# Optimization experiments

Measured on AMD Instinct MI355X. Metric: run time of the kernel, lower is better.

Reference implementation:

```python
import jax, jax.numpy as jnp
import numpy as np

F_DIM = 128; HID = 32; C = 8 * HID; DEPTH = 5; K = 3; HEADS = 8
JK_H = (7 * C) // 2  # 896, PyG JumpingKnowledge('lstm', C, jk_depth=7)
FLEX = 512; CLASSES = 10; GATE_H = 21 * HID
BS = 512; NPG = 23; N_NODES = BS * NPG
EPS = 1e-5


def _bn(x, gamma=None, beta=None):
    # training-mode BatchNorm1d (biased variance), affine optional
    mu = x.mean(0)
    var = x.var(0)
    y = (x - mu) * jax.lax.rsqrt(var + EPS)
    return y * gamma + beta if gamma is not None else y


def _lstm(seq, w_ih, w_hh, b_ih, b_hh):
    # seq: [T, N, C] -> hidden states [T, N, H]; torch gate order i,f,g,o
    n = seq.shape[1]
    hdim = w_hh.shape[1]
    def step(carry, xt):
        h, c = carry
        z = xt @ w_ih.T + h @ w_hh.T + b_ih + b_hh
        i, f, g, o = jnp.split(z, 4, axis=-1)
        c = jax.nn.sigmoid(f) * c + jax.nn.sigmoid(i) * jnp.tanh(g)
        h = jax.nn.sigmoid(o) * jnp.tanh(c)
        return (h, c), h
    init = (jnp.zeros((n, hdim), seq.dtype), jnp.zeros((n, hdim), seq.dtype))
    _, hs = jax.lax.scan(step, init, seq)
    return hs


def _forward(x, conv1_w, conv1_b, bn1_g, bn1_b, ll1_w, ll1_b, tag_w, tag_b,
             gat_w, gat_asrc, gat_adst, gat_b,
             lw_ih_f, lw_hh_f, lb_ih_f, lb_hh_f, lw_ih_b, lw_hh_b, lb_ih_b, lb_hh_b,
             jk_w, jk_b, fff_w1, fff_b1, fff_w2, fff_b2,
             gate_w1, gate_b1, gate_w2, gate_b2,
             conv2_w, conv2_b, bn2_g, bn2_b, fc_w, fc_b,
             edge_index, batch, num_graphs):
    n, f = x.shape
    bs = num_graphs
    # --- temporal preprocessing: PE over node axis (d_model=23), Conv1d, BN ---
    xt = x.reshape(bs, NPG, f).transpose(0, 2, 1)            # [bs, F, 23]
    pos = jnp.arange(f, dtype=x.dtype)[:, None]
    div = jnp.exp(jnp.arange(0, NPG, 2, dtype=x.dtype) * (-np.log(10000.0) / NPG))
    pe = jnp.zeros((f, NPG), x.dtype)
    pe = pe.at[:, 0::2].set(jnp.sin(pos * div))
    pe = pe.at[:, 1::2].set(jnp.cos(pos * div)[:, :(NPG - 1) // 2])
    xt = (xt + pe[None]).transpose(0, 2, 1)                  # [bs, 23, F]
    xt = jax.lax.conv_general_dilated(xt, conv1_w, (1,), [(1, 1)],
            dimension_numbers=('NCH', 'OIH', 'NCH')) + conv1_b[None, :, None]
    h = _bn(xt.reshape(n, f), bn1_g, bn1_b) @ ll1_w + ll1_b  # [N, HID]
    # --- symmetric gcn_norm (no self loops) shared by all TAGConv layers ---
    src, dst = edge_index[0], edge_index[1]
    deg = jax.ops.segment_sum(jnp.ones(src.shape, h.dtype), dst, n)
    dinv = jnp.where(deg > 0, jax.lax.rsqrt(jnp.maximum(deg, 1.0)), 0.0)
    wnorm = dinv[src] * dinv[dst]                            # [E]
    # GAT uses self loops
    loop = jnp.arange(n, dtype=src.dtype)
    src_sl = jnp.concatenate([src, loop])
    dst_sl = jnp.concatenate([dst, loop])

    jk_seq = []
    for i in range(DEPTH):
        # TAGConv: concat powers of normalized adjacency, then linear
        xs = h
        feats = [h]
        for _ in range(K):
            xs = jax.ops.segment_sum(wnorm[:, None] * xs[src], dst, n)
            feats.append(xs)
        tag = jnp.concatenate(feats, axis=-1) @ tag_w[i] + tag_b[i]
        h = _bn(h + tag)                                     # SublayerConnection (BN affine=False)
        # GATConv, heads=8, concat
        g = (h @ gat_w[i]).reshape(n, HEADS, HID)
        a = jax.nn.leaky_relu((g * gat_asrc[i]).sum(-1)[src_sl]
                              + (g * gat_adst[i]).sum(-1)[dst_sl], 0.2)  # [E', heads]
        m = jax.lax.stop_gradient(jax.ops.segment_max(a, dst_sl, n))
        ea = jnp.exp(a - m[dst_sl])
        alpha = ea / jax.ops.segment_sum(ea, dst_sl, n)[dst_sl]
        out = jax.ops.segment_sum(alpha[:, :, None] * g[src_sl], dst_sl, n)
        jk_seq.append(out.reshape(n, C) + gat_b[i])

    # JumpingKnowledge 'lstm': bi-LSTM attention over the DEPTH layer outputs
    seq = jnp.stack(jk_seq, axis=0)                          # [T=5, N, C]
    hf = _lstm(seq, lw_ih_f, lw_hh_f, lb_ih_f, lb_hh_f)
    hb = _lstm(seq[::-1], lw_ih_b, lw_hh_b, lb_ih_b, lb_hh_b)[::-1]
    att = (jnp.concatenate([hf, hb], -1) @ jk_w + jk_b)[..., 0]  # [T, N]
    w_jk = jax.nn.softmax(att, axis=0)                       # softmax over layers
    xg = (seq * w_jk[:, :, None]).sum(0)                     # [N, C]
    # FinalFeedForward + residual BN (slc4)
    ff = jax.nn.elu(xg @ fff_w1 + fff_b1) @ fff_w2 + fff_b2
    xg = _bn(xg + ff)
    # GlobalAttention pooling per graph
    gate = ((xg @ gate_w1 + gate_b1) @ gate_w2 + gate_b2)[:, 0]  # [N]
    gm = jax.lax.stop_gradient(jax.ops.segment_max(gate, batch, bs))
    ge = jnp.exp(gate - gm[batch])
    gw = ge / jax.ops.segment_sum(ge, batch, bs)[batch]
    pooled = jax.ops.segment_sum(gw[:, None] * xg, batch, bs)    # [bs, C]
    # Conv1d(1->10, k=9) over channel axis, mean over out-channels, BN, classifier
    y = jax.lax.conv_general_dilated(pooled[:, None, :], conv2_w, (1,), [(4, 4)],
            dimension_numbers=('NCH', 'OIH', 'NCH')) + conv2_b[None, :, None]
    y = _bn(y.mean(axis=1), bn2_g, bn2_b)
    return jax.nn.log_softmax(y @ fc_w + fc_b, axis=1)


def setup_inputs() -> dict:
    key = jax.random.key(0)
    it = iter(jax.random.split(key, 48))
    def rn(shape, scale=0.05):
        return jax.random.normal(next(it), shape, dtype=jnp.float32) * scale
    # complete digraph (no self loops) inside each 23-node graph
    s, d = np.meshgrid(np.arange(NPG), np.arange(NPG), indexing='ij')
    mask = s != d
    s, d = s[mask], d[mask]
    off = (np.arange(BS) * NPG)[:, None]
    src = (off + s[None, :]).reshape(-1)
    dst = (off + d[None, :]).reshape(-1)
    edge_index = jnp.asarray(np.stack([src, dst]), dtype=jnp.int32)
    batch = jnp.repeat(jnp.arange(BS, dtype=jnp.int32), NPG)
    return dict(
        x=rn((N_NODES, F_DIM), 1.0),
        edge_index=edge_index, batch=batch, num_graphs=BS,
        conv1_w=rn((NPG, NPG, 3)), conv1_b=rn((NPG,)),
        bn1_g=jnp.ones((F_DIM,), jnp.float32), bn1_b=jnp.zeros((F_DIM,), jnp.float32),
        ll1_w=rn((F_DIM, HID)), ll1_b=rn((HID,)),
        tag_w=rn((DEPTH, (K + 1) * HID, HID)), tag_b=rn((DEPTH, HID)),
        gat_w=rn((DEPTH, HID, HEADS * HID)), gat_asrc=rn((DEPTH, HEADS, HID)),
        gat_adst=rn((DEPTH, HEADS, HID)), gat_b=rn((DEPTH, HEADS * HID)),
        lw_ih_f=rn((4 * JK_H, C)), lw_hh_f=rn((4 * JK_H, JK_H)),
        lb_ih_f=rn((4 * JK_H,)), lb_hh_f=rn((4 * JK_H,)),
        lw_ih_b=rn((4 * JK_H, C)), lw_hh_b=rn((4 * JK_H, JK_H)),
        lb_ih_b=rn((4 * JK_H,)), lb_hh_b=rn((4 * JK_H,)),
        jk_w=rn((2 * JK_H, 1)), jk_b=rn((1,)),
        fff_w1=rn((C, FLEX)), fff_b1=rn((FLEX,)),
        fff_w2=rn((FLEX, C)), fff_b2=rn((C,)),
        gate_w1=rn((C, GATE_H)), gate_b1=rn((GATE_H,)),
        gate_w2=rn((GATE_H, 1)), gate_b2=rn((1,)),
        conv2_w=rn((10, 1, 9)), conv2_b=rn((10,)),
        bn2_g=jnp.ones((C,), jnp.float32), bn2_b=jnp.zeros((C,), jnp.float32),
        fc_w=rn((C, CLASSES)), fc_b=rn((CLASSES,)),
    )


def reference(x, edge_index, batch, num_graphs, conv1_w, conv1_b, bn1_g, bn1_b,
              ll1_w, ll1_b, tag_w, tag_b, gat_w, gat_asrc, gat_adst, gat_b,
              lw_ih_f, lw_hh_f, lb_ih_f, lb_hh_f, lw_ih_b, lw_hh_b, lb_ih_b, lb_hh_b,
              jk_w, jk_b, fff_w1, fff_b1, fff_w2, fff_b2,
              gate_w1, gate_b1, gate_w2, gate_b2,
              conv2_w, conv2_b, bn2_g, bn2_b, fc_w, fc_b):
    return _forward(x, conv1_w, conv1_b, bn1_g, bn1_b, ll1_w, ll1_b, tag_w, tag_b,
                    gat_w, gat_asrc, gat_adst, gat_b,
                    lw_ih_f, lw_hh_f, lb_ih_f, lb_hh_f, lw_ih_b, lw_hh_b, lb_ih_b, lb_hh_b,
                    jk_w, jk_b, fff_w1, fff_b1, fff_w2, fff_b2,
                    gate_w1, gate_b1, gate_w2, gate_b2,
                    conv2_w, conv2_b, bn2_g, bn2_b, fc_w, fc_b,
                    edge_index, batch, num_graphs)
```

## Files before the change

### kernel.cpp

```cpp
#include <hip/hip_runtime.h>
#include <math.h>

#define NNODES 11776
#define NGR    512
#define NPG    23
#define FDIM   128
#define HID    32
#define CDIM   256
#define JKH    896
#define ZCOLS  3584
#define EPSBN  1e-5f

typedef long long i64;
typedef unsigned short ushort_t;
typedef __attribute__((ext_vector_type(8))) short bf16x8;
typedef __attribute__((ext_vector_type(4))) float f32x4;

__device__ __forceinline__ float fsig(float x) { return 1.f / (1.f + __expf(-x)); }
__device__ __forceinline__ float ftanh(float x) {
  x = fminf(fmaxf(x, -15.f), 15.f);
  float e = __expf(2.f * x);
  return (e - 1.f) / (e + 1.f);
}

__device__ __forceinline__ ushort_t f2bf(float x) {
  unsigned u = __float_as_uint(x);
  return (ushort_t)((u + 0x7fffu + ((u >> 16) & 1u)) >> 16);
}
__device__ __forceinline__ float bf2f(ushort_t b) {
  return __uint_as_float(((unsigned)b) << 16);
}

__device__ __forceinline__ void gload16(const ushort_t* g, ushort_t* l) {
  __builtin_amdgcn_global_load_lds(
      (const __attribute__((address_space(1))) void*)g,
      (__attribute__((address_space(3))) void*)l, 16, 0, 0);
}

__global__ __launch_bounds__(256) void conv1_kernel(
    const float* __restrict__ x, const float* __restrict__ w,
    const float* __restrict__ bias, float* __restrict__ out,
    float* __restrict__ stats) {
  int b = blockIdx.x;
  __shared__ float in[NPG][FDIM];
  __shared__ float wsh[NPG * NPG * 3];
  __shared__ float cs[FDIM], cq[FDIM];
  int tid = threadIdx.x;
  if (tid < FDIM) { cs[tid] = 0.f; cq[tid] = 0.f; }
  const float c0 = -2.f * logf(10000.f) / 23.f;
  for (int idx = tid; idx < NPG * FDIM; idx += 256) {
    int p = idx >> 7, f = idx & 127;
    int j = p >> 1;
    float ang = (float)f * expf(c0 * (float)j);
    float pe = (p & 1) ? cosf(ang) : sinf(ang);
    in[p][f] = x[(i64)(b * NPG + p) * FDIM + f] + pe;
  }
  for (int idx = tid; idx < NPG * NPG * 3; idx += 256) wsh[idx] = w[idx];
  __syncthreads();
  float ls = 0.f, lq = 0.f;
  int fme = tid & 127;
  for (int idx = tid; idx < NPG * FDIM; idx += 256) {
    int o = idx >> 7, f = idx & 127;
    float acc = bias[o];
    for (int i = 0; i < NPG; ++i) {
      const float* wr = &wsh[(o * NPG + i) * 3];
      float s = in[i][f] * wr[1];
      if (f > 0)   s += in[i][f - 1] * wr[0];
      if (f < 127) s += in[i][f + 1] * wr[2];
      acc += s;
    }
    out[(i64)(b * NPG + o) * FDIM + f] = acc;
    ls += acc; lq += acc * acc;
  }
  atomicAdd(&cs[fme], ls);
  atomicAdd(&cq[fme], lq);
  __syncthreads();
  if (tid < FDIM) {
    atomicAdd(&stats[tid], cs[tid]);
    atomicAdd(&stats[FDIM + tid], cq[tid]);
  }
}

__global__ __launch_bounds__(256) void col_stats(
    const float* __restrict__ X, int rows, int cols, float* __restrict__ acc) {
  int rpt = 256 / cols;
  int c = threadIdx.x % cols;
  int rsub = threadIdx.x / cols;
  float s = 0.f, q = 0.f;
  for (int r0 = blockIdx.x * rpt; r0 < rows; r0 += gridDim.x * rpt) {
    int r = r0 + rsub;
    if (r < rows) {
      float v = X[(i64)r * cols + c];
      s += v; q += v * v;
    }
  }
  __shared__ float sh[256];
  sh[threadIdx.x] = s;
  __syncthreads();
  if (threadIdx.x < cols) {
    float t = 0.f;
    for (int g = 0; g < rpt; ++g) t += sh[g * cols + c];
    atomicAdd(&acc[c], t);
  }
  __syncthreads();
  sh[threadIdx.x] = q;
  __syncthreads();
  if (threadIdx.x < cols) {
    float t = 0.f;
    for (int g = 0; g < rpt; ++g) t += sh[g * cols + c];
    atomicAdd(&acc[cols + c], t);
  }
}

__global__ __launch_bounds__(256) void fold_ll1(
    const float* __restrict__ acc, const float* __restrict__ g,
    const float* __restrict__ be, const float* __restrict__ w,
    const float* __restrict__ lb, float* __restrict__ Wp, float* __restrict__ bp) {
  int tid = threadIdx.x;
  const float invR = 1.f / (float)NNODES;
  for (int idx = tid; idx < FDIM * HID; idx += 256) {
    int k = idx >> 5;
    float mu = acc[k] * invR;
    float var = acc[FDIM + k] * invR - mu * mu;
    float scale = g[k] * rsqrtf(var + EPSBN);
    Wp[idx] = scale * w[idx];
  }
  if (tid < HID) {
    float s = lb[tid];
    for (int k = 0; k < FDIM; ++k) {
      float mu = acc[k] * invR;
      float var = acc[FDIM + k] * invR - mu * mu;
      float scale = g[k] * rsqrtf(var + EPSBN);
      s += (be[k] - mu * scale) * w[k * HID + tid];
    }
    bp[tid] = s;
  }
}

template <int BT>
__global__ __launch_bounds__(256) void sgemm(
    const float* __restrict__ A, const float* __restrict__ B, float* __restrict__ C,
    int M, int N, int K,
    const float* __restrict__ bias, const float* __restrict__ resid,
    int act, int accumulate) {
  __shared__ float As[16][128];
  __shared__ float Bs[16][128];
  int tid = threadIdx.x;
  int bm0 = blockIdx.x * 128;
  int bn0 = blockIdx.y * 128;
  int tx = tid & 15, ty = tid >> 4;
  float acc[8][8];
#pragma unroll
  for (int i = 0; i < 8; ++i)
#pragma unroll
    for (int j = 0; j < 8; ++j) acc[i][j] = 0.f;

  int ar = tid >> 2;
  int akc = (tid & 3) << 2;
  bool bfull = (bn0 + 127 < N);

  for (int k0 = 0; k0 < K; k0 += 16) {
    {
      const float* ap = A + (i64)(bm0 + ar) * K + k0 + akc;
      float4 a0 = *(const float4*)ap;
      float4 a1 = *(const float4*)(ap + (i64)64 * K);
      As[akc + 0][ar] = a0.x; As[akc + 1][ar] = a0.y;
      As[akc + 2][ar] = a0.z; As[akc + 3][ar] = a0.w;
      As[akc + 0][ar + 64] = a1.x; As[akc + 1][ar + 64] = a1.y;
      As[akc + 2][ar + 64] = a1.z; As[akc + 3][ar + 64] = a1.w;
    }
    if (BT) {
      int br = tid >> 1;
      int bkc = (tid & 1) << 3;
      const float* bp = B + (i64)(bn0 + br) * K + k0 + bkc;
      float4 b0 = *(const float4*)bp;
      float4 b1 = *(const float4*)(bp + 4);
      Bs[bkc + 0][br] = b0.x; Bs[bkc + 1][br] = b0.y;
      Bs[bkc + 2][br] = b0.z; Bs[bkc + 3][br] = b0.w;
      Bs[bkc + 4][br] = b1.x; Bs[bkc + 5][br] = b1.y;
      Bs[bkc + 6][br] = b1.z; Bs[bkc + 7][br] = b1.w;
    } else {
      int bk = tid >> 4;
      int bn = (tid & 15) << 3;
      const float* bp = B + (i64)(k0 + bk) * N + bn0 + bn;
      if (bfull) {
        *(float4*)&Bs[bk][bn] = *(const float4*)bp;
        *(float4*)&Bs[bk][bn + 4] = *(const float4*)(bp + 4);
      } else {
#pragma unroll
        for (int q = 0; q < 8; ++q)
          Bs[bk][bn + q] = (bn0 + bn + q < N) ? bp[q] : 0.f;
      }
    }
    __syncthreads();
#pragma unroll
    for (int kk = 0; kk < 16; ++kk) {
      float a[8], b[8];
      *(float4*)(a)     = *(const float4*)&As[kk][ty * 8];
      *(float4*)(a + 4) = *(const float4*)&As[kk][ty * 8 + 4];
      *(float4*)(b)     = *(const float4*)&Bs[kk][tx * 8];
      *(float4*)(b + 4) = *(const float4*)&Bs[kk][tx * 8 + 4];
#pragma unroll
      for (int i = 0; i < 8; ++i)
#pragma unroll
        for (int j = 0; j < 8; ++j)
          acc[i][j] = fmaf(a[i], b[j], acc[i][j]);
    }
    __syncthreads();
  }
#pragma unroll
  for (int i = 0; i < 8; ++i) {
    int m = bm0 + ty * 8 + i;
#pragma unroll
    for (int j = 0; j < 8; ++j) {
      int n = bn0 + tx * 8 + j;
      if (n < N) {
        i64 ci = (i64)m * N + n;
        float v = acc[i][j];
        if (accumulate) {
          C[ci] += v;
        } else {
          if (bias) v += bias[n];
          if (act == 1) v = v > 0.f ? v : expm1f(v);
          if (resid) v += resid[ci];
          C[ci] = v;
        }
      }
    }
  }
}

__global__ __launch_bounds__(256) void tag_fused(
    const float* __restrict__ hbuf, const float* __restrict__ tag_w,
    const float* __restrict__ tag_b, float* __restrict__ hres,
    float* __restrict__ stats) {
  int b = blockIdx.x, tid = threadIdx.x;
  __shared__ float fe[NPG][FDIM];
  __shared__ float wsh[FDIM * HID];
  __shared__ float S[HID];
  __shared__ float cs[HID], cq[HID];
  if (tid < HID) { cs[tid] = 0.f; cq[tid] = 0.f; }
  const float* hp = hbuf + (i64)b * NPG * HID;
  for (int idx = tid; idx < NPG * HID; idx += 256) fe[idx >> 5][idx & 31] = hp[idx];
  for (int idx = tid; idx < FDIM * HID; idx += 256) wsh[idx] = tag_w[idx];
  __syncthreads();
  if (tid < HID) {
    float s = 0.f;
    for (int p = 0; p < NPG; ++p) s += fe[p][tid];
    S[tid] = s;
  }
  __syncthreads();
  const float wn = 1.f / 22.f;
  for (int idx = tid; idx < NPG * HID; idx += 256) {
    int p = idx >> 5, c = idx & 31;
    float f0 = fe[p][c], Sc = S[c];
    float f1 = (Sc - f0) * wn;
    float f2 = (Sc - f1) * wn;
    float f3 = (Sc - f2) * wn;
    fe[p][HID + c] = f1;
    fe[p][2 * HID + c] = f2;
    fe[p][3 * HID + c] = f3;
  }
  __syncthreads();
  for (int idx = tid; idx < NPG * HID; idx += 256) {
    int p = idx >> 5, c = idx & 31;
    float acc = tag_b[c];
#pragma unroll 8
    for (int k = 0; k < FDIM; ++k) acc += fe[p][k] * wsh[k * HID + c];
    float v = fe[p][c] + acc;
    hres[(i64)(b * NPG + p) * HID + c] = v;
    atomicAdd(&cs[c], v);
    atomicAdd(&cq[c], v * v);
  }
  __syncthreads();
  if (tid < HID) {
    atomicAdd(&stats[tid], cs[tid]);
    atomicAdd(&stats[HID + tid], cq[tid]);
  }
}

__global__ __launch_bounds__(256) void gat_tag_fused(
    const float* __restrict__ hres, const float* __restrict__ stats,
    const float* __restrict__ gat_w, const float* __restrict__ asrc,
    const float* __restrict__ adst, const float* __restrict__ gbias,
    ushort_t* __restrict__ outseq,
    const float* __restrict__ tag_w_next, const float* __restrict__ tag_b_next,
    float* __restrict__ hres_out, float* __restrict__ stats_next, int has_next) {
  int b = blockIdx.x, tid = threadIdx.x;
  __shared__ float hn[NPG * HID];
  __shared__ float ssrc[NPG * 8], sdst[NPG * 8], sinv[NPG * 8];
  __shared__ float buf[10120];
  __shared__ float S[HID], cs[HID], cq[HID];
  float* gsh = buf;
  float* ealpha = buf + 5888;
  const float invR = 1.f / (float)NNODES;
  for (int idx = tid; idx < NPG * HID; idx += 256) {
    int c = idx & 31;
    float mu = stats[c] * invR;
    float var = stats[HID + c] * invR - mu * mu;
    hn[idx] = (hres[(i64)b * NPG * HID + idx] - mu) * rsqrtf(var + EPSBN);
  }
  __syncthreads();
  for (int idx = tid; idx < NPG * CDIM; idx += 256) {
    int p = idx >> 8, d = idx & 255;
    float acc = 0.f;
#pragma unroll
    for (int k = 0; k < HID; ++k) acc += hn[p * HID + k] * gat_w[k * CDIM + d];
    gsh[idx] = acc;
  }
  __syncthreads();
  if (tid < NPG * 8) {
    int p = tid >> 3, hd = tid & 7;
    float s1 = 0.f, s2 = 0.f;
    const float* gp = &gsh[p * CDIM + hd * 32];
#pragma unroll
    for (int d = 0; d < 32; ++d) {
      s1 += gp[d] * asrc[hd * 32 + d];
      s2 += gp[d] * adst[hd * 32 + d];
    }
    ssrc[tid] = s1;
    sdst[tid] = s2;
  }
  __syncthreads();
  if (tid < NPG * 8) {
    int v = tid >> 3, hd = tid & 7;
    float sd = sdst[v * 8 + hd];
    float e[NPG];
    float m = -1e30f;
#pragma unroll
    for (int u = 0; u < NPG; ++u) {
      float xv = ssrc[u * 8 + hd] + sd;
      xv = xv > 0.f ? xv : 0.2f * xv;
      e[u] = xv;
      m = fmaxf(m, xv);
    }
    float s = 0.f;
#pragma unroll
    for (int u = 0; u < NPG; ++u) {
      float t = __expf(e[u] - m);
      ealpha[(v * NPG + u) * 8 + hd] = t;
      s += t;
    }
    sinv[tid] = 1.f / s;
  }
  __syncthreads();
  {
    int hd = tid >> 5, d = tid & 31;
    const i64 base = (i64)b * NPG * CDIM;
    for (int v = 0; v < NPG; ++v) {
      float acc = 0.f;
#pragma unroll
      for (int u = 0; u < NPG; ++u)
        acc += ealpha[(v * NPG + u) * 8 + hd] * gsh[u * CDIM + hd * 32 + d];
      outseq[base + (i64)v * CDIM + hd * 32 + d] =
          f2bf(acc * sinv[v * 8 + hd] + gbias[hd * 32 + d]);
    }
  }
  if (!has_next) return;
  __syncthreads();
  float* fe = buf;
  float* wsh = buf + 2944;
  if (tid < HID) { cs[tid] = 0.f; cq[tid] = 0.f; }
  for (int idx = tid; idx < FDIM * HID; idx += 256) wsh[idx] = tag_w_next[idx];
  for (int idx = tid; idx < NPG * HID; idx += 256)
    fe[(idx >> 5) * FDIM + (idx & 31)] = hn[idx];
  __syncthreads();
  if (tid < HID) {
    float s = 0.f;
    for (int p = 0; p < NPG; ++p) s += fe[p * FDIM + tid];
    S[tid] = s;
  }
  __syncthreads();
  const float wn = 1.f / 22.f;
  for (int idx = tid; idx < NPG * HID; idx += 256) {
    int p = idx >> 5, c = idx & 31;
    float f0 = fe[p * FDIM + c], Sc = S[c];
    float f1 = (Sc - f0) * wn;
    float f2 = (Sc - f1) * wn;
    float f3 = (Sc - f2) * wn;
    fe[p * FDIM + HID + c] = f1;
    fe[p * FDIM + 2 * HID + c] = f2;
    fe[p * FDIM + 3 * HID + c] = f3;
  }
  __syncthreads();
  for (int idx = tid; idx < NPG * HID; idx += 256) {
    int p = idx >> 5, c = idx & 31;
    float acc = tag_b_next[c];
#pragma unroll 8
    for (int k = 0; k < FDIM; ++k) acc += fe[p * FDIM + k] * wsh[k * HID + c];
    float v = fe[p * FDIM + c] + acc;
    hres_out[(i64)(b * NPG + p) * HID + c] = v;
    atomicAdd(&cs[c], v);
    atomicAdd(&cq[c], v * v);
  }
  __syncthreads();
  if (tid < HID) {
    atomicAdd(&stats_next[tid], cs[tid]);
    atomicAdd(&stats_next[HID + tid], cq[tid]);
  }
}

__global__ void pack_w(const float* __restrict__ w, ushort_t* __restrict__ wp,
                       int ldK) {
  i64 total = (i64)ZCOLS * ldK;
  i64 idx = (i64)blockIdx.x * 256 + threadIdx.x;
  i64 stride = (i64)gridDim.x * 256;
  for (; idx < total; idx += stride) {
    int r = (int)(idx / ldK), k = (int)(idx % ldK);
    int g = r / JKH, jj = r % JKH;
    int p = (jj >> 4) * 64 + g * 16 + (jj & 15);
    wp[(i64)p * ldK + k] = f2bf(w[idx]);
  }
}

__global__ void pack_b(const float* __restrict__ a, const float* __restrict__ b,
                       float* __restrict__ bp) {
  int r = blockIdx.x * 256 + threadIdx.x;
  if (r < ZCOLS) {
    int g = r / JKH, jj = r % JKH;
    int p = (jj >> 4) * 64 + g * 16 + (jj & 15);
    bp[p] = a[r] + b[r];
  }
}

__global__ void pack_t(const float* __restrict__ w, ushort_t* __restrict__ wt,
                       int K, int N) {
  i64 total = (i64)K * N;
  i64 idx = (i64)blockIdx.x * 256 + threadIdx.x;
  i64 stride = (i64)gridDim.x * 256;
  for (; idx < total; idx += stride) {
    int k = (int)(idx / N), n = (int)(idx % N);
    wt[(i64)n * K + k] = f2bf(w[idx]);
  }
}

template <int HASH>
__global__ __launch_bounds__(256) void lstm_step(
    const ushort_t* __restrict__ Aseq,
    const ushort_t* __restrict__ Wih,
    const ushort_t* __restrict__ Hprev,
    const ushort_t* __restrict__ Whh,
    const float*  __restrict__ bspk,
    float* __restrict__ Cst,
    ushort_t* __restrict__ Hout,
    const float* __restrict__ jkw,
    float* __restrict__ attp) {
  __shared__ ushort_t As[128 * 64];
  __shared__ ushort_t Bs[128 * 64];
  __shared__ float att_s[128];
  int tid = threadIdx.x;
  int w = tid >> 6, lane = tid & 63;
  int m0 = blockIdx.x * 128;
  int n0 = blockIdx.y * 128;
  f32x4 acc[4][4];
#pragma unroll
  for (int a = 0; a < 4; ++a)
#pragma unroll
    for (int b = 0; b < 4; ++b) acc[a][b] = (f32x4){0.f, 0.f, 0.f, 0.f};

  const ushort_t* aptr = Aseq;
  const ushort_t* bptr = Wih;
  int lda = CDIM, K = CDIM;
  for (int phase = 0; phase < (HASH ? 2 : 1); ++phase) {
    for (int k0 = 0; k0 < K; k0 += 64) {
#pragma unroll
      for (int i = 0; i < 4; ++i) {
        int r = w + i * 4;
        int s = r * 64 + lane;
        int row = s >> 3;
        int kc = (s & 7) ^ (row & 7);
        gload16(aptr + (i64)(m0 + row) * lda + k0 + kc * 8, &As[r * 512]);
        gload16(bptr + (i64)(n0 + row) * lda + k0 + kc * 8, &Bs[r * 512]);
      }
      __syncthreads();
#pragma unroll
      for (int ks = 0; ks < 2; ++ks) {
        bf16x8 af[4], bfr[4];
        int kq = ks * 4 + (lane >> 4);
#pragma unroll
        for (int mi = 0; mi < 4; ++mi) {
          int row = (w & 1) * 64 + mi * 16 + (lane & 15);
          int pos = row * 8 + (kq ^ (row & 7));
          af[mi] = *(const bf16x8*)&As[pos * 8];
        }
#pragma unroll
        for (int ni = 0; ni < 4; ++ni) {
          int row = (w >> 1) * 64 + ni * 16 + (lane & 15);
          int pos = row * 8 + (kq ^ (row & 7));
          bfr[ni] = *(const bf16x8*)&Bs[pos * 8];
        }
#pragma unroll
        for (int mi = 0; mi < 4; ++mi)
#pragma unroll
          for (int ni = 0; ni < 4; ++ni)
            acc[mi][ni] = __builtin_amdgcn_mfma_f32_16x16x32_bf16(
                af[mi], bfr[ni], acc[mi][ni], 0, 0, 0);
      }
      __syncthreads();
    }
    aptr = Hprev; bptr = Whh; lda = JKH; K = JKH;
  }

  if (tid < 128) att_s[tid] = 0.f;
  __syncthreads();

  int jb = (n0 >> 6) + (w >> 1);
  int j = jb * 16 + (lane & 15);
  float jw = jkw[j];
  float bsi = bspk[jb * 64 + (lane & 15)];
  float bsf = bspk[jb * 64 + 16 + (lane & 15)];
  float bsg = bspk[jb * 64 + 32 + (lane & 15)];
  float bso = bspk[jb * 64 + 48 + (lane & 15)];
#pragma unroll
  for (int mi = 0; mi < 4; ++mi) {
#pragma unroll
    for (int reg = 0; reg < 4; ++reg) {
      int mloc = (w & 1) * 64 + mi * 16 + (lane >> 4) * 4 + reg;
      int m = m0 + mloc;
      float zi = acc[mi][0][reg] + bsi;
      float zf = acc[mi][1][reg] + bsf;
      float zg = acc[mi][2][reg] + bsg;
      float zo = acc[mi][3][reg] + bso;
      i64 ci = (i64)m * JKH + j;
      float cv = fsig(zi) * ftanh(zg);
      if (HASH) cv += fsig(zf) * Cst[ci];
      Cst[ci] = cv;
      float hv = fsig(zo) * ftanh(cv);
      Hout[ci] = f2bf(hv);
      float av = hv * jw;
      av += __shfl_xor(av, 1, 64);
      av += __shfl_xor(av, 2, 64);
      av += __shfl_xor(av, 4, 64);
      av += __shfl_xor(av, 8, 64);
      if ((lane & 15) == 0) atomicAdd(&att_s[mloc], av);
    }
  }
  __syncthreads();
  if (tid < 128) atomicAdd(&attp[m0 + tid], att_s[tid]);
}

template <int ACT, int BF16OUT, int STATS>
__global__ __launch_bounds__(256) void mfma_gemm(
    const ushort_t* __restrict__ A, const ushort_t* __restrict__ Bt, int K,
    const float* __restrict__ bias, const float* __restrict__ resid,
    float* __restrict__ Cf, ushort_t* __restrict__ Cb, int N,
    float* __restrict__ stats) {
  __shared__ ushort_t As[128 * 64];
  __shared__ ushort_t Bs[128 * 64];
  __shared__ float cs[128], cq[128];
  int tid = threadIdx.x;
  int w = tid >> 6, lane = tid & 63;
  int m0 = blockIdx.x * 128;
  int n0 = blockIdx.y * 128;
  f32x4 acc[4][4];
#pragma unroll
  for (int a = 0; a < 4; ++a)
#pragma unroll
    for (int b = 0; b < 4; ++b) acc[a][b] = (f32x4){0.f, 0.f, 0.f, 0.f};

  for (int k0 = 0; k0 < K; k0 += 64) {
#pragma unroll
    for (int i = 0; i < 4; ++i) {
      int r = w + i * 4;
      int s = r * 64 + lane;
      int row = s >> 3;
      int kc = (s & 7) ^ (row & 7);
      gload16(A + (i64)(m0 + row) * K + k0 + kc * 8, &As[r * 512]);
      gload16(Bt + (i64)(n0 + row) * K + k0 + kc * 8, &Bs[r * 512]);
    }
    __syncthreads();
#pragma unroll
    for (int ks = 0; ks < 2; ++ks) {
      bf16x8 af[4], bfr[4];
      int kq = ks * 4 + (lane >> 4);
#pragma unroll
      for (int mi = 0; mi < 4; ++mi) {
        int row = (w & 1) * 64 + mi * 16 + (lane & 15);
        int pos = row * 8 + (kq ^ (row & 7));
        af[mi] = *(const bf16x8*)&As[pos * 8];
      }
#pragma unroll
      for (int ni = 0; ni < 4; ++ni) {
        int row = (w >> 1) * 64 + ni * 16 + (lane & 15);
        int pos = row * 8 + (kq ^ (row & 7));
        bfr[ni] = *(const bf16x8*)&Bs[pos * 8];
      }
#pragma unroll
      for (int mi = 0; mi < 4; ++mi)
#pragma unroll
        for (int ni = 0; ni < 4; ++ni)
          acc[mi][ni] = __builtin_amdgcn_mfma_f32_16x16x32_bf16(
              af[mi], bfr[ni], acc[mi][ni], 0, 0, 0);
    }
    __syncthreads();
  }
  if (STATS) {
    if (tid < 128) { cs[tid] = 0.f; cq[tid] = 0.f; }
    __syncthreads();
  }
#pragma unroll
  for (int ni = 0; ni < 4; ++ni) {
    int nloc = (w >> 1) * 64 + ni * 16 + (lane & 15);
    int n = n0 + nloc;
    float bv = bias[n];
    float s = 0.f, q = 0.f;
#pragma unroll
    for (int mi = 0; mi < 4; ++mi) {
#pragma unroll
      for (int reg = 0; reg < 4; ++reg) {
        int m = m0 + (w & 1) * 64 + mi * 16 + (lane >> 4) * 4 + reg;
        float v = acc[mi][ni][reg] + bv;
        if (ACT) v = v > 0.f ? v : expm1f(v);
        i64 ci = (i64)m * N + n;
        if (BF16OUT) Cb[ci] = f2bf(v);
        else {
          v += resid[ci];
          Cf[ci] = v;
          if (STATS) { s += v; q += v * v; }
        }
      }
    }
    if (STATS) { atomicAdd(&cs[nloc], s); atomicAdd(&cq[nloc], q); }
  }
  if (STATS) {
    __syncthreads();
    if (tid < 128) {
      atomicAdd(&stats[n0 + tid], cs[tid]);
      atomicAdd(&stats[N + n0 + tid], cq[tid]);
    }
  }
}

__global__ __launch_bounds__(256) void jk_combine(const float* __restrict__ att,
                                                  const ushort_t* __restrict__ seq,
                                                  float* __restrict__ xg,
                                                  ushort_t* __restrict__ xgb) {
  int n = blockIdx.x, c = threadIdx.x;
  float a[5];
  float m = -1e30f;
#pragma unroll
  for (int t = 0; t < 5; ++t) {
    a[t] = att[(i64)t * NNODES + n] + att[(i64)(5 + t) * NNODES + n];
    m = fmaxf(m, a[t]);
  }
  float s = 0.f;
#pragma unroll
  for (int t = 0; t < 5; ++t) { a[t] = __expf(a[t] - m); s += a[t]; }
  float inv = 1.f / s;
  float acc = 0.f;
#pragma unroll
  for (int t = 0; t < 5; ++t)
    acc += bf2f(seq[((i64)t * NNODES + n) * CDIM + c]) * (a[t] * inv);
  xg[(i64)n * CDIM + c] = acc;
  xgb[(i64)n * CDIM + c] = f2bf(acc);
}

__global__ void fill0(float* __restrict__ p, i64 nfloat) {
  i64 i = (i64)blockIdx.x * 256 + threadIdx.x;
  i64 stride = (i64)gridDim.x * 256;
  for (; i < nfloat; i += stride) p[i] = 0.f;
}

__global__ __launch_bounds__(256) void fold_gate(
    const float* __restrict__ w1, const float* __restrict__ b1,
    const float* __restrict__ w2, const float* __restrict__ b2,
    float* __restrict__ v, float* __restrict__ b0) {
  int tid = threadIdx.x;
  float s = 0.f;
  for (int j = 0; j < 672; ++j) s += w1[tid * 672 + j] * w2[j];
  v[tid] = s;
  float p = 0.f;
  for (int j = tid; j < 672; j += 256) p += b1[j] * w2[j];
  __shared__ float sh[4];
#pragma unroll
  for (int o = 32; o > 0; o >>= 1) p += __shfl_down(p, o, 64);
  if ((tid & 63) == 0) sh[tid >> 6] = p;
  __syncthreads();
  if (tid == 0) b0[0] = sh[0] + sh[1] + sh[2] + sh[3] + b2[0];
}

__global__ __launch_bounds__(256) void pool_kernel(
    const float* __restrict__ s4, const float* __restrict__ st,
    const float* __restrict__ v, const float* __restrict__ b0,
    float* __restrict__ pooled) {
  int g = blockIdx.x, tid = threadIdx.x;
  __shared__ float xn[NPG][CDIM];
  __shared__ float gw[NPG];
  __shared__ float sh[4];
  const float invR = 1.f / (float)NNODES;
  float mu = st[tid] * invR;
  float var = st[CDIM + tid] * invR - mu * mu;
  float rs = rsqrtf(var + EPSBN);
  for (int p = 0; p < NPG; ++p)
    xn[p][tid] = (s4[(i64)(g * NPG + p) * CDIM + tid] - mu) * rs;
  __syncthreads();
  float myv = v[tid];
  for (int p = 0; p < NPG; ++p) {
    float val = xn[p][tid] * myv;
#pragma unroll
    for (int o = 32; o > 0; o >>= 1) val += __shfl_down(val, o, 64);
    if ((tid & 63) == 0) sh[tid >> 6] = val;
    __syncthreads();
    if (tid == 0) gw[p] = sh[0] + sh[1] + sh[2] + sh[3] + b0[0];
    __syncthreads();
  }
  if (tid == 0) {
    float m = -1e30f;
    for (int p = 0; p < NPG; ++p) m = fmaxf(m, gw[p]);
    float s = 0.f;
    for (int p = 0; p < NPG; ++p) { gw[p] = __expf(gw[p] - m); s += gw[p]; }
    float inv = 1.f / s;
    for (int p = 0; p < NPG; ++p) gw[p] *= inv;
  }
  __syncthreads();
  float acc = 0.f;
  for (int p = 0; p < NPG; ++p) acc += gw[p] * xn[p][tid];
  pooled[(i64)g * CDIM + tid] = acc;
}

__global__ void fold_conv2(const float* __restrict__ w, const float* __restrict__ b,
                           float* __restrict__ wbar) {
  int tid = threadIdx.x;
  if (tid < 9) {
    float s = 0.f;
    for (int o = 0; o < 10; ++o) s += w[o * 9 + tid];
    wbar[tid] = s * 0.1f;
  } else if (tid == 9) {
    float s = 0.f;
    for (int o = 0; o < 10; ++o) s += b[o];
    wbar[9] = s * 0.1f;
  }
}

__global__ __launch_bounds__(256) void conv2mean(const float* __restrict__ pooled,
                                                 const float* __restrict__ wbar,
                                                 float* __restrict__ y2) {
  int b = blockIdx.x, h = threadIdx.x;
  __shared__ float row[CDIM];
  row[h] = pooled[(i64)b * CDIM + h];
  __syncthreads();
  float s = wbar[9];
#pragma unroll
  for (int t = 0; t < 9; ++t) {
    int hh = h + t - 4;
    if (hh >= 0 && hh < CDIM) s += row[hh] * wbar[t];
  }
  y2[(i64)b * CDIM + h] = s;
}

__global__ __launch_bounds__(256) void final_fc(
    const float* __restrict__ y2, const float* __restrict__ acc,
    const float* __restrict__ g2, const float* __restrict__ b2,
    const float* __restrict__ fcw, const float* __restrict__ fcb,
    float* __restrict__ out) {
  int b = blockIdx.x, tid = threadIdx.x;
  __shared__ float yn[CDIM];
  __shared__ float logits[10];
  __shared__ float red[2];
  float mu = acc[tid] / 512.f;
  float var = acc[CDIM + tid] / 512.f - mu * mu;
  yn[tid] = (y2[(i64)b * CDIM + tid] - mu) * rsqrtf(var + EPSBN) * g2[tid] + b2[tid];
  __syncthreads();
  if (tid < 10) {
    float s = fcb[tid];
    for (int h = 0; h < CDIM; ++h) s += yn[h] * fcw[h * 10 + tid];
    logits[tid] = s;
  }
  __syncthreads();
  if (tid == 0) {
    float m = -1e30f;
    for (int o = 0; o < 10; ++o) m = fmaxf(m, logits[o]);
    float s = 0.f;
    for (int o = 0; o < 10; ++o) s += expf(logits[o] - m);
    red[0] = m;
    red[1] = logf(s);
  }
  __syncthreads();
  if (tid < 10) out[(i64)b * 10 + tid] = logits[tid] - red[0] - red[1];
}

extern "C" void kernel_launch(void* const* d_in, const int* in_sizes, int n_in,
                              void* d_out, int out_size, void* d_ws, size_t ws_size,
                              hipStream_t stream) {
  (void)in_sizes; (void)n_in; (void)out_size;
  const float* x        = (const float*)d_in[0];
  const float* conv1_w  = (const float*)d_in[4];
  const float* conv1_b  = (const float*)d_in[5];
  const float* bn1_g    = (const float*)d_in[6];
  const float* bn1_b    = (const float*)d_in[7];
  const float* ll1_w    = (const float*)d_in[8];
  const float* ll1_b    = (const float*)d_in[9];
  const float* tag_w    = (const float*)d_in[10];
  const float* tag_b    = (const float*)d_in[11];
  const float* gat_w    = (const float*)d_in[12];
  const float* gat_asrc = (const float*)d_in[13];
  const float* gat_adst = (const float*)d_in[14];
  const float* gat_b    = (const float*)d_in[15];
  const float* lw_ih[2] = {(const float*)d_in[16], (const float*)d_in[20]};
  const float* lw_hh[2] = {(const float*)d_in[17], (const float*)d_in[21]};
  const float* lb_ih[2] = {(const float*)d_in[18], (const float*)d_in[22]};
  const float* lb_hh[2] = {(const float*)d_in[19], (const float*)d_in[23]};
  const float* jk_w     = (const float*)d_in[24];
  const float* fff_w1   = (const float*)d_in[26];
  const float* fff_b1   = (const float*)d_in[27];
  const float* fff_w2   = (const float*)d_in[28];
  const float* fff_b2   = (const float*)d_in[29];
  const float* gate_w1  = (const float*)d_in[30];
  const float* gate_b1  = (const float*)d_in[31];
  const float* gate_w2  = (const float*)d_in[32];
  const float* gate_b2  = (const float*)d_in[33];
  const float* conv2_w  = (const float*)d_in[34];
  const float* conv2_b  = (const float*)d_in[35];
  const float* bn2_g    = (const float*)d_in[36];
  const float* bn2_b    = (const float*)d_in[37];
  const float* fc_w     = (const float*)d_in[38];
  const float* fc_b     = (const float*)d_in[39];
  float* out = (float*)d_out;

  float* ws = (float*)d_ws;
  i64 off = 0;
  auto alloc = [&](i64 n) { float* p = ws + off; off += (n + 15) & ~(i64)15; return p; };
  ushort_t* seqb = (ushort_t*)alloc(7536640);
  float* att = alloc(10 * NNODES);
  float* st1 = alloc(256);
  float* st2 = alloc(6 * 64);
  float* st4 = alloc(512);
  float* st5 = alloc(512);
  i64 zcount = (i64)(st5 - att) + 512;
  float* xg     = alloc((i64)NNODES * CDIM);
  ushort_t* xgb = (ushort_t*)alloc((i64)NNODES * CDIM / 2);
  float* hbuf   = alloc((i64)NNODES * HID);
  float* hres   = alloc((i64)NNODES * HID);
  float* Wp     = alloc(FDIM * HID);
  float* bp     = alloc(64);
  ushort_t* wihb[2]; ushort_t* whhb[2]; float* bspk[2];
  for (int d = 0; d < 2; ++d) {
    wihb[d] = (ushort_t*)alloc((i64)ZCOLS * CDIM / 2);
    whhb[d] = (ushort_t*)alloc((i64)ZCOLS * JKH / 2);
    bspk[d] = alloc(ZCOLS);
  }
  ushort_t* w1t = (ushort_t*)alloc(512 * 256 / 2);
  ushort_t* w2t = (ushort_t*)alloc(256 * 512 / 2);
  float* gatev  = alloc(CDIM);
  float* gateb0 = alloc(16);
  float* wbar   = alloc(16);
  float* pooled = alloc((i64)NGR * CDIM);
  float* y2     = alloc((i64)NGR * CDIM);
  float* Zs = ws + off;
  i64 S = (i64)(ws_size / 4) - off;
  if (S < 0) S = 0;

  int Tch = (int)(S / 172032); if (Tch < 1) Tch = 1; if (Tch > 92) Tch = 92;
  i64 Sff = S - 3014656;
  int Tf = (int)(Sff / 32768); if (Tf < 1) Tf = 1; if (Tf > 92) Tf = 92;

  float* xconv = Zs;
  ushort_t* hA = (ushort_t*)Zs;
  ushort_t* hB = hA + (i64)Tch * 128 * JKH;
  float* cch   = (float*)(hB + (i64)Tch * 128 * JKH);
  float* s4  = Zs;
  ushort_t* ff1b = (ushort_t*)(s4 + 3014656);

  fill0<<<512, 256, 0, stream>>>(att, zcount);
  for (int d = 0; d < 2; ++d) {
    pack_w<<<2048, 256, 0, stream>>>(lw_ih[d], wihb[d], CDIM);
    pack_w<<<4096, 256, 0, stream>>>(lw_hh[d], whhb[d], JKH);
    pack_b<<<14, 256, 0, stream>>>(lb_ih[d], lb_hh[d], bspk[d]);
  }
  pack_t<<<512, 256, 0, stream>>>(fff_w1, w1t, CDIM, 512);
  pack_t<<<512, 256, 0, stream>>>(fff_w2, w2t, 512, CDIM);

  conv1_kernel<<<NGR, 256, 0, stream>>>(x, conv1_w, conv1_b, xconv, st1);
  fold_ll1<<<1, 256, 0, stream>>>(st1, bn1_g, bn1_b, ll1_w, ll1_b, Wp, bp);
  sgemm<0><<<dim3(92, 1), 256, 0, stream>>>(xconv, Wp, hbuf, NNODES, HID, FDIM,
                                            bp, nullptr, 0, 0);

  tag_fused<<<NGR, 256, 0, stream>>>(hbuf, tag_w, tag_b, hres, st2);
  for (int i = 0; i < 5; ++i) {
    int nx = (i < 4) ? (i + 1) : 0;
    gat_tag_fused<<<NGR, 256, 0, stream>>>(
        hres, st2 + i * 64, gat_w + (i64)i * HID * CDIM,
        gat_asrc + i * 256, gat_adst + i * 256, gat_b + i * 256,
        seqb + (i64)i * NNODES * CDIM,
        tag_w + (i64)nx * FDIM * HID, tag_b + nx * HID,
        hres, st2 + (i + 1) * 64, (i < 4) ? 1 : 0);
  }

  for (int dir = 0; dir < 2; ++dir) {
    for (int t0 = 0; t0 < 92; t0 += Tch) {
      int tiles = (92 - t0 < Tch) ? (92 - t0) : Tch;
      i64 r0 = (i64)t0 * 128;
      ushort_t* hp[2] = {hA, hB};
      for (int t = 0; t < 5; ++t) {
        int ts = dir ? 4 - t : t;
        const ushort_t* Ax = seqb + ((i64)ts * NNODES + r0) * CDIM;
        float* attp = att + (i64)(dir * 5 + ts) * NNODES + r0;
        if (t == 0)
          lstm_step<0><<<dim3(tiles, 28), 256, 0, stream>>>(
              Ax, wihb[dir], nullptr, nullptr, bspk[dir], cch, hp[0],
              jk_w + dir * JKH, attp);
        else
          lstm_step<1><<<dim3(tiles, 28), 256, 0, stream>>>(
              Ax, wihb[dir], hp[(t + 1) & 1], whhb[dir], bspk[dir], cch, hp[t & 1],
              jk_w + dir * JKH, attp);
      }
    }
  }
  jk_combine<<<NNODES, 256, 0, stream>>>(att, seqb, xg, xgb);

  for (int t0 = 0; t0 < 92; t0 += Tf) {
    int tiles = (92 - t0 < Tf) ? (92 - t0) : Tf;
    i64 r0 = (i64)t0 * 128;
    mfma_gemm<1, 1, 0><<<dim3(tiles, 4), 256, 0, stream>>>(
        xgb + r0 * CDIM, w1t, CDIM, fff_b1, nullptr, nullptr, ff1b, 512, nullptr);
    mfma_gemm<0, 0, 1><<<dim3(tiles, 2), 256, 0, stream>>>(
        ff1b, w2t, 512, fff_b2, xg + r0 * CDIM, s4 + r0 * CDIM, nullptr, CDIM, st4);
  }

  fold_gate<<<1, 256, 0, stream>>>(gate_w1, gate_b1, gate_w2, gate_b2, gatev, gateb0);
  pool_kernel<<<NGR, 256, 0, stream>>>(s4, st4, gatev, gateb0, pooled);
  fold_conv2<<<1, 64, 0, stream>>>(conv2_w, conv2_b, wbar);
  conv2mean<<<NGR, 256, 0, stream>>>(pooled, wbar, y2);
  col_stats<<<64, 256, 0, stream>>>(y2, NGR, CDIM, st5);
  final_fc<<<NGR, 256, 0, stream>>>(y2, st5, bn2_g, bn2_b, fc_w, fc_b, out);
}
```

Measured before the change: 1.674 ms.

## Run LSTM GEMMs in FP8 and merge small prep kernels

Converts the bidirectional LSTM step GEMMs from bf16 to fp8 (e4m3) MFMA. Weights, the input sequence and the hidden states are now stored as fp8, and the cell state is kept in bf16. This halves operand bytes and doubles MFMA throughput per instruction, at the cost of precision and an extra fp8 copy of the GAT output. It also merges the gate, conv2 and bias folding into one prep kernel and computes the BN2 column stats with atomics inside conv2mean, which removes several launches.

```diff
diff --git a/kernel.cpp b/kernel.cpp
--- a/kernel.cpp
+++ b/kernel.cpp
@@ -13,6 +13,7 @@
 
 typedef long long i64;
 typedef unsigned short ushort_t;
+typedef unsigned char u8;
 typedef __attribute__((ext_vector_type(8))) short bf16x8;
 typedef __attribute__((ext_vector_type(4))) float f32x4;
 
@@ -31,7 +32,33 @@
   return __uint_as_float(((unsigned)b) << 16);
 }
 
+__device__ __forceinline__ u8 f2fp8(float x) {
+  unsigned u = __float_as_uint(x);
+  unsigned sign = (u >> 24) & 0x80u;
+  float ax = fabsf(x);
+  if (ax > 448.f) return (u8)(sign | 0x7e);
+  if (ax < 0.0009765625f) return (u8)sign;
+  int e = (int)((u >> 23) & 0xff) - 127;
+  if (e < -6) {
+    int mi = (int)rintf(ax * 512.f);
+    return (u8)(sign | (unsigned)mi);
+  }
+  unsigned m = u & 0x7fffffu;
+  unsigned mant = m >> 20;
+  unsigned rest = m & 0xfffffu;
+  if (rest > 0x80000u || (rest == 0x80000u && (mant & 1u))) mant++;
+  unsigned exp = (unsigned)(e + 7);
+  if (mant == 8u) { mant = 0u; exp++; }
+  if (exp > 15u || (exp == 15u && mant == 7u)) return (u8)(sign | 0x7e);
+  return (u8)(sign | (exp << 3) | mant);
+}
+
 __device__ __forceinline__ void gload16(const ushort_t* g, ushort_t* l) {
+  __builtin_amdgcn_global_load_lds(
+      (const __attribute__((address_space(1))) void*)g,
+      (__attribute__((address_space(3))) void*)l, 16, 0, 0);
+}
+__device__ __forceinline__ void gload16b(const u8* g, u8* l) {
   __builtin_amdgcn_global_load_lds(
       (const __attribute__((address_space(1))) void*)g,
       (__attribute__((address_space(3))) void*)l, 16, 0, 0);
@@ -78,37 +105,6 @@
   if (tid < FDIM) {
     atomicAdd(&stats[tid], cs[tid]);
     atomicAdd(&stats[FDIM + tid], cq[tid]);
-  }
-}
-
-__global__ __launch_bounds__(256) void col_stats(
-    const float* __restrict__ X, int rows, int cols, float* __restrict__ acc) {
-  int rpt = 256 / cols;
-  int c = threadIdx.x % cols;
-  int rsub = threadIdx.x / cols;
-  float s = 0.f, q = 0.f;
-  for (int r0 = blockIdx.x * rpt; r0 < rows; r0 += gridDim.x * rpt) {
-    int r = r0 + rsub;
-    if (r < rows) {
-      float v = X[(i64)r * cols + c];
-      s += v; q += v * v;
-    }
-  }
-  __shared__ float sh[256];
-  sh[threadIdx.x] = s;
-  __syncthreads();
-  if (threadIdx.x < cols) {
-    float t = 0.f;
-    for (int g = 0; g < rpt; ++g) t += sh[g * cols + c];
-    atomicAdd(&acc[c], t);
-  }
-  __syncthreads();
-  sh[threadIdx.x] = q;
-  __syncthreads();
-  if (threadIdx.x < cols) {
-    float t = 0.f;
-    for (int g = 0; g < rpt; ++g) t += sh[g * cols + c];
-    atomicAdd(&acc[cols + c], t);
   }
 }
 
@@ -283,7 +279,7 @@
     const float* __restrict__ hres, const float* __restrict__ stats,
     const float* __restrict__ gat_w, const float* __restrict__ asrc,
     const float* __restrict__ adst, const float* __restrict__ gbias,
-    ushort_t* __restrict__ outseq,
+    ushort_t* __restrict__ outseq, u8* __restrict__ outseq8,
     const float* __restrict__ tag_w_next, const float* __restrict__ tag_b_next,
     float* __restrict__ hres_out, float* __restrict__ stats_next, int has_next) {
   int b = blockIdx.x, tid = threadIdx.x;
@@ -352,8 +348,10 @@
 #pragma unroll
       for (int u = 0; u < NPG; ++u)
         acc += ealpha[(v * NPG + u) * 8 + hd] * gsh[u * CDIM + hd * 32 + d];
-      outseq[base + (i64)v * CDIM + hd * 32 + d] =
-          f2bf(acc * sinv[v * 8 + hd] + gbias[hd * 32 + d]);
+      float val = acc * sinv[v * 8 + hd] + gbias[hd * 32 + d];
+      i64 oi = base + (i64)v * CDIM + hd * 32 + d;
+      outseq[oi] = f2bf(val);
+      outseq8[oi] = f2fp8(val);
     }
   }
   if (!has_next) return;
@@ -400,8 +398,8 @@
   }
 }
 
-__global__ void pack_w(const float* __restrict__ w, ushort_t* __restrict__ wp,
-                       int ldK) {
+__global__ void pack_w8(const float* __restrict__ w, u8* __restrict__ wp,
+                        int ldK) {
   i64 total = (i64)ZCOLS * ldK;
   i64 idx = (i64)blockIdx.x * 256 + threadIdx.x;
   i64 stride = (i64)gridDim.x * 256;
@@ -409,17 +407,7 @@
     int r = (int)(idx / ldK), k = (int)(idx % ldK);
     int g = r / JKH, jj = r % JKH;
     int p = (jj >> 4) * 64 + g * 16 + (jj & 15);
-    wp[(i64)p * ldK + k] = f2bf(w[idx]);
-  }
-}
-
-__global__ void pack_b(const float* __restrict__ a, const float* __restrict__ b,
-                       float* __restrict__ bp) {
-  int r = blockIdx.x * 256 + threadIdx.x;
-  if (r < ZCOLS) {
-    int g = r / JKH, jj = r % JKH;
-    int p = (jj >> 4) * 64 + g * 16 + (jj & 15);
-    bp[p] = a[r] + b[r];
+    wp[(i64)p * ldK + k] = f2fp8(w[idx]);
   }
 }
 
@@ -434,19 +422,63 @@
   }
 }
 
+__global__ __launch_bounds__(256) void small_prep(
+    const float* __restrict__ gw1, const float* __restrict__ gb1,
+    const float* __restrict__ gw2, const float* __restrict__ gb2,
+    float* __restrict__ gatev, float* __restrict__ gateb0,
+    const float* __restrict__ cw, const float* __restrict__ cb,
+    float* __restrict__ wbar,
+    const float* __restrict__ bi0, const float* __restrict__ bh0,
+    float* __restrict__ bp0,
+    const float* __restrict__ bi1, const float* __restrict__ bh1,
+    float* __restrict__ bp1) {
+  int blk = blockIdx.x, tid = threadIdx.x;
+  if (blk == 0) {
+    float s = 0.f;
+    for (int j = 0; j < 672; ++j) s += gw1[tid * 672 + j] * gw2[j];
+    gatev[tid] = s;
+    float p = 0.f;
+    for (int j = tid; j < 672; j += 256) p += gb1[j] * gw2[j];
+    __shared__ float sh[4];
+#pragma unroll
+    for (int o = 32; o > 0; o >>= 1) p += __shfl_down(p, o, 64);
+    if ((tid & 63) == 0) sh[tid >> 6] = p;
+    __syncthreads();
+    if (tid == 0) gateb0[0] = sh[0] + sh[1] + sh[2] + sh[3] + gb2[0];
+  } else if (blk == 1) {
+    if (tid < 9) {
+      float s = 0.f;
+      for (int o = 0; o < 10; ++o) s += cw[o * 9 + tid];
+      wbar[tid] = s * 0.1f;
+    } else if (tid == 9) {
+      float s = 0.f;
+      for (int o = 0; o < 10; ++o) s += cb[o];
+      wbar[9] = s * 0.1f;
+    }
+  } else {
+    for (int r = (blk - 2) * 256 + tid; r < 2 * ZCOLS; r += 15 * 256) {
+      int d = r / ZCOLS, rr = r % ZCOLS;
+      int g = rr / JKH, jj = rr % JKH;
+      int p = (jj >> 4) * 64 + g * 16 + (jj & 15);
+      if (d == 0) bp0[p] = bi0[rr] + bh0[rr];
+      else        bp1[p] = bi1[rr] + bh1[rr];
+    }
+  }
+}
+
 template <int HASH>
-__global__ __launch_bounds__(256) void lstm_step(
-    const ushort_t* __restrict__ Aseq,
-    const ushort_t* __restrict__ Wih,
-    const ushort_t* __restrict__ Hprev,
-    const ushort_t* __restrict__ Whh,
-    const float*  __restrict__ bspk,
-    float* __restrict__ Cst,
-    ushort_t* __restrict__ Hout,
+__global__ __launch_bounds__(256) void lstm_step8(
+    const u8* __restrict__ Aseq,
+    const u8* __restrict__ Wih,
+    const u8* __restrict__ Hprev,
+    const u8* __restrict__ Whh,
+    const float* __restrict__ bspk,
+    ushort_t* __restrict__ Cst,
+    u8* __restrict__ Hout,
     const float* __restrict__ jkw,
     float* __restrict__ attp) {
-  __shared__ ushort_t As[128 * 64];
-  __shared__ ushort_t Bs[128 * 64];
+  __shared__ u8 As[128 * 64];
+  __shared__ u8 Bs[128 * 64];
   __shared__ float att_s[128];
   int tid = threadIdx.x;
   int w = tid >> 6, lane = tid & 63;
@@ -458,42 +490,41 @@
 #pragma unroll
     for (int b = 0; b < 4; ++b) acc[a][b] = (f32x4){0.f, 0.f, 0.f, 0.f};
 
-  const ushort_t* aptr = Aseq;
-  const ushort_t* bptr = Wih;
+  const u8* aptr = Aseq;
+  const u8* bptr = Wih;
   int lda = CDIM, K = CDIM;
   for (int phase = 0; phase < (HASH ? 2 : 1); ++phase) {
     for (int k0 = 0; k0 < K; k0 += 64) {
 #pragma unroll
-      for (int i = 0; i < 4; ++i) {
+      for (int i = 0; i < 2; ++i) {
         int r = w + i * 4;
-        int s = r * 64 + lane;
-        int row = s >> 3;
-        int kc = (s & 7) ^ (row & 7);
-        gload16(aptr + (i64)(m0 + row) * lda + k0 + kc * 8, &As[r * 512]);
-        gload16(bptr + (i64)(n0 + row) * lda + k0 + kc * 8, &Bs[r * 512]);
+        int row = r * 16 + (lane >> 2);
+        int kc = (lane & 3) ^ ((row >> 1) & 3);
+        gload16b(aptr + (i64)(m0 + row) * lda + k0 + kc * 16, &As[r * 1024]);
+        gload16b(bptr + (i64)(n0 + row) * lda + k0 + kc * 16, &Bs[r * 1024]);
       }
       __syncthreads();
 #pragma unroll
       for (int ks = 0; ks < 2; ++ks) {
-        bf16x8 af[4], bfr[4];
+        long af[4], bfr[4];
         int kq = ks * 4 + (lane >> 4);
 #pragma unroll
         for (int mi = 0; mi < 4; ++mi) {
           int row = (w & 1) * 64 + mi * 16 + (lane & 15);
-          int pos = row * 8 + (kq ^ (row & 7));
-          af[mi] = *(const bf16x8*)&As[pos * 8];
+          int off = row * 64 + (((kq >> 1) ^ ((row >> 1) & 3)) << 4) + ((kq & 1) << 3);
+          af[mi] = *(const long*)&As[off];
         }
 #pragma unroll
         for (int ni = 0; ni < 4; ++ni) {
           int row = (w >> 1) * 64 + ni * 16 + (lane & 15);
-          int pos = row * 8 + (kq ^ (row & 7));
-          bfr[ni] = *(const bf16x8*)&Bs[pos * 8];
+          int off = row * 64 + (((kq >> 1) ^ ((row >> 1) & 3)) << 4) + ((kq & 1) << 3);
+          bfr[ni] = *(const long*)&Bs[off];
         }
 #pragma unroll
         for (int mi = 0; mi < 4; ++mi)
 #pragma unroll
           for (int ni = 0; ni < 4; ++ni)
-            acc[mi][ni] = __builtin_amdgcn_mfma_f32_16x16x32_bf16(
+            acc[mi][ni] = __builtin_amdgcn_mfma_f32_16x16x32_fp8_fp8(
                 af[mi], bfr[ni], acc[mi][ni], 0, 0, 0);
       }
       __syncthreads();
@@ -523,10 +554,10 @@
       float zo = acc[mi][3][reg] + bso;
       i64 ci = (i64)m * JKH + j;
       float cv = fsig(zi) * ftanh(zg);
-      if (HASH) cv += fsig(zf) * Cst[ci];
-      Cst[ci] = cv;
+      if (HASH) cv += fsig(zf) * bf2f(Cst[ci]);
+      Cst[ci] = f2bf(cv);
       float hv = fsig(zo) * ftanh(cv);
-      Hout[ci] = f2bf(hv);
+      Hout[ci] = f2fp8(hv);
       float av = hv * jw;
       av += __shfl_xor(av, 1, 64);
       av += __shfl_xor(av, 2, 64);
@@ -661,24 +692,6 @@
   for (; i < nfloat; i += stride) p[i] = 0.f;
 }
 
-__global__ __launch_bounds__(256) void fold_gate(
-    const float* __restrict__ w1, const float* __restrict__ b1,
-    const float* __restrict__ w2, const float* __restrict__ b2,
-    float* __restrict__ v, float* __restrict__ b0) {
-  int tid = threadIdx.x;
-  float s = 0.f;
-  for (int j = 0; j < 672; ++j) s += w1[tid * 672 + j] * w2[j];
-  v[tid] = s;
-  float p = 0.f;
-  for (int j = tid; j < 672; j += 256) p += b1[j] * w2[j];
-  __shared__ float sh[4];
-#pragma unroll
-  for (int o = 32; o > 0; o >>= 1) p += __shfl_down(p, o, 64);
-  if ((tid & 63) == 0) sh[tid >> 6] = p;
-  __syncthreads();
-  if (tid == 0) b0[0] = sh[0] + sh[1] + sh[2] + sh[3] + b2[0];
-}
-
 __global__ __launch_bounds__(256) void pool_kernel(
     const float* __restrict__ s4, const float* __restrict__ st,
     const float* __restrict__ v, const float* __restrict__ b0,
@@ -718,23 +731,10 @@
   pooled[(i64)g * CDIM + tid] = acc;
 }
 
-__global__ void fold_conv2(const float* __restrict__ w, const float* __restrict__ b,
-                           float* __restrict__ wbar) {
-  int tid = threadIdx.x;
-  if (tid < 9) {
-    float s = 0.f;
-    for (int o = 0; o < 10; ++o) s += w[o * 9 + tid];
-    wbar[tid] = s * 0.1f;
-  } else if (tid == 9) {
-    float s = 0.f;
-    for (int o = 0; o < 10; ++o) s += b[o];
-    wbar[9] = s * 0.1f;
-  }
-}
-
 __global__ __launch_bounds__(256) void conv2mean(const float* __restrict__ pooled,
                                                  const float* __restrict__ wbar,
-                                                 float* __restrict__ y2) {
+                                                 float* __restrict__ y2,
+                                                 float* __restrict__ st5) {
   int b = blockIdx.x, h = threadIdx.x;
   __shared__ float row[CDIM];
   row[h] = pooled[(i64)b * CDIM + h];
@@ -746,6 +746,8 @@
     if (hh >= 0 && hh < CDIM) s += row[hh] * wbar[t];
   }
   y2[(i64)b * CDIM + h] = s;
+  atomicAdd(&st5[h], s);
+  atomicAdd(&st5[CDIM + h], s * s);
 }
 
 __global__ __launch_bounds__(256) void final_fc(
@@ -821,6 +823,7 @@
   i64 off = 0;
   auto alloc = [&](i64 n) { float* p = ws + off; off += (n + 15) & ~(i64)15; return p; };
   ushort_t* seqb = (ushort_t*)alloc(7536640);
+  u8* seq8      = (u8*)alloc(3768320);
   float* att = alloc(10 * NNODES);
   float* st1 = alloc(256);
   float* st2 = alloc(6 * 64);
@@ -833,10 +836,10 @@
   float* hres   = alloc((i64)NNODES * HID);
   float* Wp     = alloc(FDIM * HID);
   float* bp     = alloc(64);
-  ushort_t* wihb[2]; ushort_t* whhb[2]; float* bspk[2];
+  u8* wih8[2]; u8* whh8[2]; float* bspk[2];
   for (int d = 0; d < 2; ++d) {
-    wihb[d] = (ushort_t*)alloc((i64)ZCOLS * CDIM / 2);
-    whhb[d] = (ushort_t*)alloc((i64)ZCOLS * JKH / 2);
+    wih8[d] = (u8*)alloc((i64)ZCOLS * CDIM / 4);
+    whh8[d] = (u8*)alloc((i64)ZCOLS * JKH / 4);
     bspk[d] = alloc(ZCOLS);
   }
   ushort_t* w1t = (ushort_t*)alloc(512 * 256 / 2);
@@ -850,25 +853,28 @@
   i64 S = (i64)(ws_size / 4) - off;
   if (S < 0) S = 0;
 
-  int Tch = (int)(S / 172032); if (Tch < 1) Tch = 1; if (Tch > 92) Tch = 92;
+  int Tch = (int)(S / 114688); if (Tch < 1) Tch = 1; if (Tch > 92) Tch = 92;
   i64 Sff = S - 3014656;
   int Tf = (int)(Sff / 32768); if (Tf < 1) Tf = 1; if (Tf > 92) Tf = 92;
 
   float* xconv = Zs;
-  ushort_t* hA = (ushort_t*)Zs;
-  ushort_t* hB = hA + (i64)Tch * 128 * JKH;
-  float* cch   = (float*)(hB + (i64)Tch * 128 * JKH);
+  u8* hA = (u8*)Zs;
+  u8* hB = hA + (i64)Tch * 128 * JKH;
+  ushort_t* cch = (ushort_t*)(hB + (i64)Tch * 128 * JKH);
   float* s4  = Zs;
   ushort_t* ff1b = (ushort_t*)(s4 + 3014656);
 
   fill0<<<512, 256, 0, stream>>>(att, zcount);
   for (int d = 0; d < 2; ++d) {
-    pack_w<<<2048, 256, 0, stream>>>(lw_ih[d], wihb[d], CDIM);
-    pack_w<<<4096, 256, 0, stream>>>(lw_hh[d], whhb[d], JKH);
-    pack_b<<<14, 256, 0, stream>>>(lb_ih[d], lb_hh[d], bspk[d]);
+    pack_w8<<<2048, 256, 0, stream>>>(lw_ih[d], wih8[d], CDIM);
+    pack_w8<<<4096, 256, 0, stream>>>(lw_hh[d], whh8[d], JKH);
   }
   pack_t<<<512, 256, 0, stream>>>(fff_w1, w1t, CDIM, 512);
   pack_t<<<512, 256, 0, stream>>>(fff_w2, w2t, 512, CDIM);
+  small_prep<<<17, 256, 0, stream>>>(gate_w1, gate_b1, gate_w2, gate_b2,
+                                     gatev, gateb0, conv2_w, conv2_b, wbar,
+                                     lb_ih[0], lb_hh[0], bspk[0],
+                                     lb_ih[1], lb_hh[1], bspk[1]);
 
   conv1_kernel<<<NGR, 256, 0, stream>>>(x, conv1_w, conv1_b, xconv, st1);
   fold_ll1<<<1, 256, 0, stream>>>(st1, bn1_g, bn1_b, ll1_w, ll1_b, Wp, bp);
@@ -881,7 +887,7 @@
     gat_tag_fused<<<NGR, 256, 0, stream>>>(
         hres, st2 + i * 64, gat_w + (i64)i * HID * CDIM,
         gat_asrc + i * 256, gat_adst + i * 256, gat_b + i * 256,
-        seqb + (i64)i * NNODES * CDIM,
+        seqb + (i64)i * NNODES * CDIM, seq8 + (i64)i * NNODES * CDIM,
         tag_w + (i64)nx * FDIM * HID, tag_b + nx * HID,
         hres, st2 + (i + 1) * 64, (i < 4) ? 1 : 0);
   }
@@ -890,18 +896,18 @@
     for (int t0 = 0; t0 < 92; t0 += Tch) {
       int tiles = (92 - t0 < Tch) ? (92 - t0) : Tch;
       i64 r0 = (i64)t0 * 128;
-      ushort_t* hp[2] = {hA, hB};
+      u8* hp[2] = {hA, hB};
       for (int t = 0; t < 5; ++t) {
         int ts = dir ? 4 - t : t;
-        const ushort_t* Ax = seqb + ((i64)ts * NNODES + r0) * CDIM;
+        const u8* Ax = seq8 + ((i64)ts * NNODES + r0) * CDIM;
         float* attp = att + (i64)(dir * 5 + ts) * NNODES + r0;
         if (t == 0)
-          lstm_step<0><<<dim3(tiles, 28), 256, 0, stream>>>(
-              Ax, wihb[dir], nullptr, nullptr, bspk[dir], cch, hp[0],
+          lstm_step8<0><<<dim3(tiles, 28), 256, 0, stream>>>(
+              Ax, wih8[dir], nullptr, nullptr, bspk[dir], cch, hp[0],
               jk_w + dir * JKH, attp);
         else
-          lstm_step<1><<<dim3(tiles, 28), 256, 0, stream>>>(
-              Ax, wihb[dir], hp[(t + 1) & 1], whhb[dir], bspk[dir], cch, hp[t & 1],
+          lstm_step8<1><<<dim3(tiles, 28), 256, 0, stream>>>(
+              Ax, wih8[dir], hp[(t + 1) & 1], whh8[dir], bspk[dir], cch, hp[t & 1],
               jk_w + dir * JKH, attp);
       }
     }
@@ -917,10 +923,7 @@
         ff1b, w2t, 512, fff_b2, xg + r0 * CDIM, s4 + r0 * CDIM, nullptr, CDIM, st4);
   }
 
-  fold_gate<<<1, 256, 0, stream>>>(gate_w1, gate_b1, gate_w2, gate_b2, gatev, gateb0);
   pool_kernel<<<NGR, 256, 0, stream>>>(s4, st4, gatev, gateb0, pooled);
-  fold_conv2<<<1, 64, 0, stream>>>(conv2_w, conv2_b, wbar);
-  conv2mean<<<NGR, 256, 0, stream>>>(pooled, wbar, y2);
-  col_stats<<<64, 256, 0, stream>>>(y2, NGR, CDIM, st5);
+  conv2mean<<<NGR, 256, 0, stream>>>(pooled, wbar, y2, st5);
   final_fc<<<NGR, 256, 0, stream>>>(y2, st5, bn2_g, bn2_b, fc_w, fc_b, out);
 }
```

Measured after the change: 1.875 ms. 1.12x slower.
